# Kernel optimization log

Hardware: AMD Instinct MI355X
Metric: run time of the kernel (lower is better)

The kernel has to match this reference:

```python
import jax, jax.numpy as jnp
import numpy as np

WS = 7  # window size
EPS_COS = 1e-8
BN_EPS = 1e-5


def _third_layer_mask():
    row = np.repeat(np.arange(7), 7)[:14]
    b = np.tile(row, (7, 1))                      # (7,14) values {0,1}
    m = np.concatenate([b, b + 2], axis=0)        # (14,14) values {0,1,2,3}
    return jnp.asarray(m, dtype=jnp.int32)


def _window_partition(x, ws):
    B, C, H, W = x.shape
    x = x.reshape(B, C, H // ws, ws, W // ws, ws)
    return x.transpose(0, 2, 4, 3, 5, 1).reshape(B, (H // ws) * (W // ws), ws * ws, C)


def _windows_select(x, k):
    a0 = _window_partition(x, WS)                               # (B,nW,49,C)
    nrm = jnp.linalg.norm(a0, axis=-1)                          # (B,nW,49)
    dots = jnp.einsum('bwic,bwjc->bwij', a0, a0)
    cos = dots / jnp.maximum(nrm[..., :, None] * nrm[..., None, :], EPS_COS)
    s = jnp.triu(cos).sum(axis=(-2, -1))                        # (B,nW)
    _, idx = jax.lax.top_k(s, k)                                # (B,k)
    return idx


def _spitial_sim_weight(s):
    # s: (B, N, N) attention scores, N = 196
    B, N, _ = s.shape
    spa = jnp.mean(s, axis=-1, keepdims=True)                   # (B,N,1)
    os_spa = jnp.abs(spa - jnp.swapaxes(spa, -1, -2))           # (B,N,N)
    vals, _ = jax.lax.top_k(os_spa, N // 2)                     # descending
    last = vals[..., -1:]                                       # k-th largest, (B,N,1)
    os1f = os_spa + jnp.eye(N, dtype=s.dtype) * 10000.0
    os1 = jnp.where(os1f < last, 0.0, 1.0)
    # NOTE: original code compares the *binarized* os_spa_1 against last_value
    os2 = jnp.where(os1 > last, 0.0, 1.0)
    w1 = os1 * s
    w1 = jax.nn.softmax(jnp.where(w1 == 0, -100.0, w1), axis=-1)
    w2 = os2 * s
    w2 = jax.nn.softmax(jnp.where(w2 == 0, -100.0, w2), axis=-1)
    return w1 + w2


def _conv1x1(x, w, b):
    return jnp.einsum('bchw,oc->bohw', x, w) + b[None, :, None, None]


def _conv3x3(x, w, b):
    y = jax.lax.conv_general_dilated(x, w, (1, 1), 'SAME',
                                     dimension_numbers=('NCHW', 'OIHW', 'NCHW'))
    return y + b[None, :, None, None]


def _bn_train(x, g, beta):
    m = x.mean(axis=(0, 2, 3), keepdims=True)
    v = x.var(axis=(0, 2, 3), keepdims=True)
    return (x - m) / jnp.sqrt(v + BN_EPS) * g[None, :, None, None] + beta[None, :, None, None]


def setup_inputs() -> dict:
    key = jax.random.key(0)
    ks = jax.random.split(key, 16)
    B, C = 256, 384
    Ch = C // 4
    sc = 0.02
    return {
        'x': jax.random.normal(ks[0], (B, C, 14, 14), jnp.float32),
        'qw': jax.random.normal(ks[1], (C, C), jnp.float32) * sc,
        'qb': jnp.zeros((C,), jnp.float32),
        'kw': jax.random.normal(ks[2], (C, C), jnp.float32) * sc,
        'kb': jnp.zeros((C,), jnp.float32),
        'vw': jax.random.normal(ks[3], (C, C), jnp.float32) * sc,
        'vb': jnp.zeros((C,), jnp.float32),
        'fcw': jax.random.normal(ks[4], (C, C), jnp.float32) * sc,
        'fcb': jnp.zeros((C,), jnp.float32),
        'c1w': jax.random.normal(ks[5], (Ch, C, 3, 3), jnp.float32) * sc,
        'c1b': jnp.zeros((Ch,), jnp.float32),
        'bn1g': jnp.ones((Ch,), jnp.float32),
        'bn1b': jnp.zeros((Ch,), jnp.float32),
        'c2w': jax.random.normal(ks[6], (C, Ch, 3, 3), jnp.float32) * sc,
        'c2b': jnp.zeros((C,), jnp.float32),
        'bn2g': jnp.ones((C,), jnp.float32),
        'bn2b': jnp.zeros((C,), jnp.float32),
        'gamm': 1,
    }


def reference(x, qw, qb, kw, kb, vw, vb, fcw, fcb,
              c1w, c1b, bn1g, bn1b, c2w, c2b, bn2g, bn2b, gamm):
    B, C, H, W = x.shape
    sel = _windows_select(x, 2)                                  # (B,2) window ids
    third = _third_layer_mask()                                  # (14,14)
    member = (third[None, :, :, None] == sel[:, None, None, :]).any(-1)  # (B,14,14)
    mask = jnp.where(member, 0.0, 1.0)[:, None]                  # (B,1,14,14)
    mask1 = 1.0 - mask
    g = jnp.asarray(gamm, x.dtype)
    mask = mask.at[0].set(g)
    mask1 = mask1.at[0].set(g)

    q = _conv1x1(x * mask, qw, qb).reshape(B, C, -1).transpose(0, 2, 1)   # (B,HW,C)
    k = _conv1x1(x * mask1, kw, kb).reshape(B, C, -1).transpose(0, 2, 1)
    v = _conv1x1(x, vw, vb).reshape(B, C, -1).transpose(0, 2, 1)

    attn = jnp.einsum('bic,bjc->bij', q, k)                      # (B,196,196)
    w = _spitial_sim_weight(attn)
    feat = jnp.einsum('bij,bjc->bic', w, v)                      # (B,196,C)
    out = feat @ fcw.T + fcb
    out = out.transpose(0, 2, 1).reshape(B, 384, 14, 14)
    out = jax.nn.relu(_bn_train(_conv3x3(out, c1w, c1b), bn1g, bn1b))
    out = jax.nn.relu(_bn_train(_conv3x3(out, c2w, c2b), bn2g, bn2b))
    return out
```

## Files before the change

kernel.cpp:

```cpp
#include <hip/hip_runtime.h>

static constexpr int B_ = 256;
static constexpr int C_ = 384;
static constexpr int N_ = 196;
static constexpr int H_ = 14;
static constexpr int CH_ = 96;
static constexpr int PW_ = 49;
static constexpr int NPAIR_ = 1225;

using bf8 = __attribute__((ext_vector_type(8))) short;
using f4  = __attribute__((ext_vector_type(4))) float;

__device__ __forceinline__ float bf2f(unsigned short u) {
    unsigned int x = ((unsigned int)u) << 16;
    return __builtin_bit_cast(float, x);
}
__device__ __forceinline__ unsigned short f2bf(float f) {
    unsigned int x = __builtin_bit_cast(unsigned int, f);
    x = x + 0x7FFFu + ((x >> 16) & 1u);
    return (unsigned short)(x >> 16);
}

__global__ __launch_bounds__(256) void k_winsel(const float* __restrict__ x,
                                                float* __restrict__ swin) {
    int blk = blockIdx.x;
    int b = blk >> 2, wi = blk & 3;
    int hr = (wi >> 1) * 7, wc0 = (wi & 1) * 7;
    __shared__ float xs[128 * PW_];
    __shared__ float dots[NPAIR_];
    __shared__ float nrm[PW_];
    __shared__ float red[256];
    int tid = threadIdx.x;
    int pi[5], pj[5];
    int nm = 0;
    for (int p = tid; p < NPAIR_; p += 256) {
        int pp = p, i = 0;
        while (pp >= PW_ - i) { pp -= PW_ - i; ++i; }
        pi[nm] = i; pj[nm] = i + pp; ++nm;
    }
    float acc[5] = {0.f, 0.f, 0.f, 0.f, 0.f};
    for (int c0 = 0; c0 < C_; c0 += 128) {
        __syncthreads();
        for (int e = tid; e < 128 * PW_; e += 256) {
            int cc = e / PW_, i = e - cc * PW_;
            int h = hr + i / 7, w = wc0 + i % 7;
            xs[e] = x[((b * C_ + c0 + cc) * H_ + h) * H_ + w];
        }
        __syncthreads();
        for (int cc = 0; cc < 128; ++cc) {
            const float* row = &xs[cc * PW_];
            #pragma unroll
            for (int t = 0; t < 5; ++t)
                if (t < nm) acc[t] = fmaf(row[pi[t]], row[pj[t]], acc[t]);
        }
    }
    for (int t = 0; t < nm; ++t) dots[tid + t * 256] = acc[t];
    __syncthreads();
    if (tid < PW_) {
        int diag = tid * PW_ - tid * (tid - 1) / 2;
        nrm[tid] = sqrtf(dots[diag]);
    }
    __syncthreads();
    float part = 0.f;
    for (int t = 0; t < nm; ++t) {
        float den = fmaxf(nrm[pi[t]] * nrm[pj[t]], 1e-8f);
        part += dots[tid + t * 256] / den;
    }
    red[tid] = part;
    __syncthreads();
    for (int st = 128; st > 0; st >>= 1) {
        if (tid < st) red[tid] += red[tid + st];
        __syncthreads();
    }
    if (tid == 0) swin[blk] = red[0];
}

__global__ __launch_bounds__(256) void k_mask(const float* __restrict__ swin,
                                              const void* __restrict__ gammp,
                                              float* __restrict__ mA,
                                              float* __restrict__ mB) {
    int b = blockIdx.x;
    float sv[4];
    #pragma unroll
    for (int i = 0; i < 4; ++i) sv[i] = swin[b * 4 + i];
    int i0 = 0; float bv = sv[0];
    #pragma unroll
    for (int i = 1; i < 4; ++i) if (sv[i] > bv) { bv = sv[i]; i0 = i; }
    int i1 = -1; float bv1 = -1e30f;
    #pragma unroll
    for (int i = 0; i < 4; ++i) {
        if (i == i0) continue;
        if (sv[i] > bv1) { bv1 = sv[i]; i1 = i; }
    }
    int iv = *(const int*)gammp;
    float g = (iv == 1) ? 1.0f : __int_as_float(iv);
    int n = threadIdx.x;
    if (n < N_) {
        int h = n / 14, w = n - h * 14;
        int widx = ((h >= 7) ? 2 : 0) + ((w >= 7) ? 1 : 0);
        bool member = (widx == i0) || (widx == i1);
        float a = member ? 0.f : 1.f;
        float bm = 1.f - a;
        if (b == 0) { a = g; bm = g; }
        mA[b * N_ + n] = a;
        mB[b * N_ + n] = bm;
    }
}

__global__ __launch_bounds__(256) void k_qkv(const float* __restrict__ x,
                                             const float* __restrict__ W,
                                             const float* __restrict__ bias,
                                             const float* __restrict__ mask,
                                             float* __restrict__ out) {
    int b = blockIdx.x, n0 = blockIdx.y * 64, o0 = blockIdx.z * 64;
    __shared__ float xs[16][65];
    __shared__ float ws[64][17];
    int tid = threadIdx.x, tx = tid & 15, ty = tid >> 4;
    float acc[4][4] = {};
    for (int c0 = 0; c0 < C_; c0 += 16) {
        __syncthreads();
        for (int e = tid; e < 1024; e += 256) {
            int cc = e >> 6, nn = e & 63;
            int n = n0 + nn;
            xs[cc][nn] = (n < N_) ? x[(b * C_ + c0 + cc) * N_ + n] : 0.f;
        }
        for (int e = tid; e < 1024; e += 256) {
            int oo = e >> 4, cc = e & 15;
            ws[oo][cc] = W[(o0 + oo) * C_ + c0 + cc];
        }
        __syncthreads();
        #pragma unroll
        for (int cc = 0; cc < 16; ++cc) {
            float a[4], bb[4];
            #pragma unroll
            for (int i = 0; i < 4; ++i) a[i] = xs[cc][ty * 4 + i];
            #pragma unroll
            for (int j = 0; j < 4; ++j) bb[j] = ws[tx * 4 + j][cc];
            #pragma unroll
            for (int i = 0; i < 4; ++i)
                #pragma unroll
                for (int j = 0; j < 4; ++j) acc[i][j] = fmaf(a[i], bb[j], acc[i][j]);
        }
    }
    #pragma unroll
    for (int i = 0; i < 4; ++i) {
        int n = n0 + ty * 4 + i;
        if (n >= N_) continue;
        float m = mask ? mask[b * N_ + n] : 1.f;
        #pragma unroll
        for (int j = 0; j < 4; ++j) {
            int o = o0 + tx * 4 + j;
            out[(b * N_ + n) * C_ + o] = m * acc[i][j] + bias[o];
        }
    }
}

__global__ __launch_bounds__(256) void k_attn(const float* __restrict__ q,
                                              const float* __restrict__ k,
                                              float* __restrict__ attn) {
    int b = blockIdx.x, i0 = blockIdx.y * 64, j0 = blockIdx.z * 64;
    __shared__ float qs[64][17];
    __shared__ float ks[64][17];
    int tid = threadIdx.x, tx = tid & 15, ty = tid >> 4;
    float acc[4][4] = {};
    for (int c0 = 0; c0 < C_; c0 += 16) {
        __syncthreads();
        for (int e = tid; e < 1024; e += 256) {
            int r = e >> 4, cc = e & 15;
            int i = i0 + r;
            qs[r][cc] = (i < N_) ? q[(b * N_ + i) * C_ + c0 + cc] : 0.f;
            int j = j0 + r;
            ks[r][cc] = (j < N_) ? k[(b * N_ + j) * C_ + c0 + cc] : 0.f;
        }
        __syncthreads();
        #pragma unroll
        for (int cc = 0; cc < 16; ++cc) {
            float a[4], bb[4];
            #pragma unroll
            for (int i = 0; i < 4; ++i) a[i] = qs[ty * 4 + i][cc];
            #pragma unroll
            for (int j = 0; j < 4; ++j) bb[j] = ks[tx * 4 + j][cc];
            #pragma unroll
            for (int i = 0; i < 4; ++i)
                #pragma unroll
                for (int j = 0; j < 4; ++j) acc[i][j] = fmaf(a[i], bb[j], acc[i][j]);
        }
    }
    #pragma unroll
    for (int i = 0; i < 4; ++i) {
        int ii = i0 + ty * 4 + i;
        if (ii >= N_) continue;
        #pragma unroll
        for (int j = 0; j < 4; ++j) {
            int jj = j0 + tx * 4 + j;
            if (jj < N_) attn[(b * N_ + ii) * N_ + jj] = acc[i][j];
        }
    }
}

__global__ __launch_bounds__(256) void k_spa(const float* __restrict__ attn,
                                             float* __restrict__ spa) {
    int row = blockIdx.x;
    const float* rp = attn + (size_t)row * N_;
    int t = threadIdx.x;
    float v = (t < N_) ? rp[t] : 0.f;
    __shared__ float red[256];
    red[t] = v; __syncthreads();
    for (int st = 128; st > 0; st >>= 1) {
        if (t < st) red[t] += red[t + st];
        __syncthreads();
    }
    if (t == 0) spa[row] = red[0] / (float)N_;
}

__global__ __launch_bounds__(256) void k_weight(const float* __restrict__ attn,
                                                const float* __restrict__ spa,
                                                unsigned short* __restrict__ wbf) {
    int row = blockIdx.x;
    int b = row / N_, i = row - b * N_;
    int t = threadIdx.x;
    __shared__ float osp[N_];
    __shared__ float red[256];
    __shared__ float lastsh;
    float myspa = spa[row];
    float o = 0.f;
    if (t < N_) { o = fabsf(myspa - spa[b * N_ + t]); osp[t] = o; }
    __syncthreads();
    if (t < N_) {
        int cgt = 0, ceq = 0;
        for (int j = 0; j < N_; ++j) {
            float oj = osp[j];
            cgt += (oj > o) ? 1 : 0;
            ceq += (oj == o) ? 1 : 0;
        }
        if (cgt <= 97 && cgt + ceq >= 98) lastsh = o;
    }
    __syncthreads();
    float last = lastsh;
    const float* rowp = attn + (size_t)row * N_;
    float s = (t < N_) ? rowp[t] : 0.f;
    float a1 = -1e30f, a2 = -1e30f;
    if (t < N_) {
        float of = o + ((t == i) ? 10000.f : 0.f);
        float o1 = (of < last) ? 0.f : 1.f;
        float o2 = (o1 > last) ? 0.f : 1.f;
        float w1 = o1 * s;
        float w2 = o2 * s;
        a1 = (w1 == 0.f) ? -100.f : w1;
        a2 = (w2 == 0.f) ? -100.f : w2;
    }
    red[t] = a1; __syncthreads();
    for (int st = 128; st > 0; st >>= 1) {
        if (t < st) red[t] = fmaxf(red[t], red[t + st]);
        __syncthreads();
    }
    float m1 = red[0]; __syncthreads();
    float e1 = (t < N_) ? expf(a1 - m1) : 0.f;
    red[t] = e1; __syncthreads();
    for (int st = 128; st > 0; st >>= 1) {
        if (t < st) red[t] += red[t + st];
        __syncthreads();
    }
    float S1 = red[0]; __syncthreads();
    red[t] = a2; __syncthreads();
    for (int st = 128; st > 0; st >>= 1) {
        if (t < st) red[t] = fmaxf(red[t], red[t + st]);
        __syncthreads();
    }
    float m2 = red[0]; __syncthreads();
    float e2 = (t < N_) ? expf(a2 - m2) : 0.f;
    red[t] = e2; __syncthreads();
    for (int st = 128; st > 0; st >>= 1) {
        if (t < st) red[t] += red[t + st];
        __syncthreads();
    }
    float S2 = red[0]; __syncthreads();
    if (t < 224)
        wbf[(size_t)row * 224 + t] = (t < N_) ? f2bf(e1 / S1 + e2 / S2) : (unsigned short)0;
}

__global__ __launch_bounds__(256) void k_wprep(const float* __restrict__ c1w,
                                               const float* __restrict__ c2w,
                                               const float* __restrict__ vw,
                                               const float* __restrict__ fcw,
                                               unsigned short* __restrict__ W1p,
                                               unsigned short* __restrict__ W2p,
                                               unsigned short* __restrict__ vwb,
                                               unsigned short* __restrict__ fcwb) {
    int i = blockIdx.x * 256 + threadIdx.x;
    if (i < 331776) {
        int qt = i >> 5, k = i & 31;
        int q = qt / (9 * 96); int r = qt - q * 9 * 96;
        int tap = r / 96, o = r - tap * 96;
        W1p[i] = f2bf(c1w[(o * 384 + q * 32 + k) * 9 + tap]);
        return;
    }
    i -= 331776;
    if (i < 331776) {
        int qt = i >> 5, k = i & 31;
        int q = qt / (9 * 384); int r = qt - q * 9 * 384;
        int tap = r / 384, o = r - tap * 384;
        W2p[i] = f2bf(c2w[(o * 96 + q * 32 + k) * 9 + tap]);
        return;
    }
    i -= 331776;
    if (i < 147456) { vwb[i] = f2bf(vw[i]); return; }
    i -= 147456;
    if (i < 147456) { fcwb[i] = f2bf(fcw[i]); }
}

template <int CIN, int COUT, bool TRANS>
__global__ __launch_bounds__(256) void k_convm(
    const unsigned short* __restrict__ in,
    const unsigned short* __restrict__ Wg,
    const float* __restrict__ cb,
    const float* __restrict__ scale,
    const float* __restrict__ shift,
    unsigned short* __restrict__ outb,
    float* __restrict__ outf,
    float* __restrict__ ssum, float* __restrict__ ssq) {
    constexpr int CPT = CIN / 32;
    __shared__ unsigned short Bs[197 * 40];
    int b = blockIdx.x, o0 = blockIdx.y * 32;
    int tid = threadIdx.x, lane = tid & 63, wid = tid >> 6;
    int col = lane & 15, rowg = lane >> 4;

    if (tid < 10) *(unsigned long long*)&Bs[196 * 40 + tid * 4] = 0ull;

    int a0[4], vb[4];
    #pragma unroll
    for (int f = 0; f < 4; ++f) {
        int px = wid * 64 + f * 16 + col;
        int h = px / 14, w = px - h * 14;
        a0[f] = px * 80 + rowg * 16;
        int m = 0;
        #pragma unroll
        for (int tap = 0; tap < 9; ++tap) {
            int dh = tap / 3 - 1, dw = tap % 3 - 1;
            if (px < 196 && (unsigned)(h + dh) < 14u && (unsigned)(w + dw) < 14u)
                m |= 1 << tap;
        }
        vb[f] = m;
    }
    const int zaddr = 196 * 80 + rowg * 16;
    const int doff[9] = {-15 * 80, -14 * 80, -13 * 80, -80, 0, 80, 13 * 80, 14 * 80, 15 * 80};

    f4 acc[4][2];
    #pragma unroll
    for (int f = 0; f < 4; ++f) { acc[f][0] = (f4){0,0,0,0}; acc[f][1] = (f4){0,0,0,0}; }

    int c4 = (tid & 7) << 2, pxs = tid >> 3;
    int cpair = tid & 15, qd0 = tid >> 4;

    for (int kq = 0; kq < CPT; ++kq) {
        __syncthreads();
        if constexpr (!TRANS) {
            #pragma unroll
            for (int i = 0; i < 7; ++i) {
                int px = pxs + 32 * i;
                if (px < 196)
                    *(unsigned long long*)&Bs[px * 40 + c4] =
                        *(const unsigned long long*)&in[((size_t)b * 196 + px) * CIN + kq * 32 + c4];
            }
        } else {
            int ch = kq * 32 + 2 * cpair;
            float s0 = scale[ch], s1 = scale[ch + 1];
            float h0 = shift[ch], h1 = shift[ch + 1];
            const unsigned short* r0 = in + ((size_t)b * CIN + ch) * 196;
            const unsigned short* r1 = r0 + 196;
            #pragma unroll
            for (int qi = 0; qi < 4; ++qi) {
                int quad = qd0 + 16 * qi;
                if (quad < 49) {
                    unsigned long long ra = *(const unsigned long long*)&r0[quad * 4];
                    unsigned long long rb = *(const unsigned long long*)&r1[quad * 4];
                    #pragma unroll
                    for (int j = 0; j < 4; ++j) {
                        float v0 = fmaxf(fmaf(bf2f((unsigned short)(ra >> (16 * j))), s0, h0), 0.f);
                        float v1 = fmaxf(fmaf(bf2f((unsigned short)(rb >> (16 * j))), s1, h1), 0.f);
                        unsigned int pk = (unsigned int)f2bf(v0) | ((unsigned int)f2bf(v1) << 16);
                        *(unsigned int*)&Bs[(quad * 4 + j) * 40 + cpair * 2] = pk;
                    }
                }
            }
        }
        __syncthreads();
        #pragma unroll
        for (int tap = 0; tap < 9; ++tap) {
            const unsigned short* wp =
                Wg + ((size_t)((kq * 9 + tap) * COUT) + o0 + col) * 32 + rowg * 8;
            bf8 af0 = *(const bf8*)wp;
            bf8 af1 = *(const bf8*)(wp + 16 * 32);
            #pragma unroll
            for (int f = 0; f < 4; ++f) {
                int ba = ((vb[f] >> tap) & 1) ? a0[f] + doff[tap] : zaddr;
                bf8 bv = *(const bf8*)((const char*)Bs + ba);
                acc[f][0] = __builtin_amdgcn_mfma_f32_16x16x32_bf16(af0, bv, acc[f][0], 0, 0, 0);
                acc[f][1] = __builtin_amdgcn_mfma_f32_16x16x32_bf16(af1, bv, acc[f][1], 0, 0, 0);
            }
        }
    }

    float bias[2][4], s1a[2][4] = {}, s2a[2][4] = {};
    #pragma unroll
    for (int oh = 0; oh < 2; ++oh)
        #pragma unroll
        for (int r = 0; r < 4; ++r) bias[oh][r] = cb[o0 + oh * 16 + rowg * 4 + r];
    #pragma unroll
    for (int f = 0; f < 4; ++f) {
        int px = wid * 64 + f * 16 + col;
        bool pv = px < 196;
        #pragma unroll
        for (int oh = 0; oh < 2; ++oh)
            #pragma unroll
            for (int r = 0; r < 4; ++r) {
                float val = acc[f][oh][r] + bias[oh][r];
                if (pv) {
                    int o = o0 + oh * 16 + rowg * 4 + r;
                    if constexpr (!TRANS)
                        outb[((size_t)b * COUT + o) * 196 + px] = f2bf(val);
                    else
                        outf[((size_t)b * COUT + o) * 196 + px] = val;
                    s1a[oh][r] += val;
                    s2a[oh][r] += val * val;
                }
            }
    }
    #pragma unroll
    for (int oh = 0; oh < 2; ++oh)
        #pragma unroll
        for (int r = 0; r < 4; ++r) {
            float a = s1a[oh][r], c = s2a[oh][r];
            #pragma unroll
            for (int m = 8; m >= 1; m >>= 1) {
                a += __shfl_xor(a, m, 64);
                c += __shfl_xor(c, m, 64);
            }
            if (col == 0) {
                int o = o0 + oh * 16 + rowg * 4 + r;
                atomicAdd(&ssum[o], a);
                atomicAdd(&ssq[o], c);
            }
        }
}

template <int K, bool BIASCOL>
__global__ __launch_bounds__(256) void k_gemm_nt(
    const unsigned short* __restrict__ A,
    const unsigned short* __restrict__ Bm, long bstrB,
    const float* __restrict__ biasc,
    unsigned short* __restrict__ out) {
    __shared__ unsigned short Bs[197 * 40];
    int b = blockIdx.x, c0 = blockIdx.y * 32;
    int tid = threadIdx.x, lane = tid & 63, wid = tid >> 6;
    int col = lane & 15, rowg = lane >> 4;
    const unsigned short* Ab = A + (size_t)b * 196 * K;
    const unsigned short* Bb = Bm + (size_t)b * bstrB;

    if (tid < 10) *(unsigned long long*)&Bs[196 * 40 + tid * 4] = 0ull;
    int a0[4]; bool pv[4];
    #pragma unroll
    for (int f = 0; f < 4; ++f) {
        int px = wid * 64 + f * 16 + col;
        a0[f] = px * 80 + rowg * 16;
        pv[f] = px < 196;
    }
    const int zaddr = 196 * 80 + rowg * 16;
    f4 acc[4][2];
    #pragma unroll
    for (int f = 0; f < 4; ++f) { acc[f][0] = (f4){0,0,0,0}; acc[f][1] = (f4){0,0,0,0}; }
    int c4 = (tid & 7) << 2, pxs = tid >> 3;

    for (int kq = 0; kq < K / 32; ++kq) {
        __syncthreads();
        #pragma unroll
        for (int i = 0; i < 7; ++i) {
            int px = pxs + 32 * i;
            if (px < 196)
                *(unsigned long long*)&Bs[px * 40 + c4] =
                    *(const unsigned long long*)&Ab[(size_t)px * K + kq * 32 + c4];
        }
        __syncthreads();
        const unsigned short* bp = Bb + (size_t)(c0 + col) * K + kq * 32 + rowg * 8;
        bf8 b0 = *(const bf8*)bp;
        bf8 b1 = *(const bf8*)(bp + (size_t)16 * K);
        #pragma unroll
        for (int f = 0; f < 4; ++f) {
            int ba = pv[f] ? a0[f] : zaddr;
            bf8 av = *(const bf8*)((const char*)Bs + ba);
            acc[f][0] = __builtin_amdgcn_mfma_f32_16x16x32_bf16(av, b0, acc[f][0], 0, 0, 0);
            acc[f][1] = __builtin_amdgcn_mfma_f32_16x16x32_bf16(av, b1, acc[f][1], 0, 0, 0);
        }
    }
    float bc[2] = {0.f, 0.f};
    if constexpr (BIASCOL) { bc[0] = biasc[c0 + col]; bc[1] = biasc[c0 + 16 + col]; }
    #pragma unroll
    for (int f = 0; f < 4; ++f) {
        #pragma unroll
        for (int oh = 0; oh < 2; ++oh)
            #pragma unroll
            for (int r = 0; r < 4; ++r) {
                int m = wid * 64 + f * 16 + rowg * 4 + r;
                if (m < 196)
                    out[((size_t)b * 196 + m) * 384 + c0 + oh * 16 + col] =
                        f2bf(acc[f][oh][r] + bc[oh]);
            }
    }
}

__global__ __launch_bounds__(256) void k_gemm_v(
    const float* __restrict__ x,
    const unsigned short* __restrict__ vwb,
    const float* __restrict__ vbias,
    unsigned short* __restrict__ vt) {
    __shared__ unsigned short Bs[197 * 40];
    int b = blockIdx.x, o0 = blockIdx.y * 32;
    int tid = threadIdx.x, lane = tid & 63, wid = tid >> 6;
    int col = lane & 15, rowg = lane >> 4;

    if (tid < 10) *(unsigned long long*)&Bs[196 * 40 + tid * 4] = 0ull;
    int a0[4]; bool pv[4];
    #pragma unroll
    for (int f = 0; f < 4; ++f) {
        int px = wid * 64 + f * 16 + col;
        a0[f] = px * 80 + rowg * 16;
        pv[f] = px < 196;
    }
    const int zaddr = 196 * 80 + rowg * 16;
    f4 acc[4][2];
    #pragma unroll
    for (int f = 0; f < 4; ++f) { acc[f][0] = (f4){0,0,0,0}; acc[f][1] = (f4){0,0,0,0}; }
    int cpair = tid & 15, qd0 = tid >> 4;

    for (int kq = 0; kq < 12; ++kq) {
        __syncthreads();
        const float* r0 = x + ((size_t)b * 384 + kq * 32 + 2 * cpair) * 196;
        const float* r1 = r0 + 196;
        #pragma unroll
        for (int qi = 0; qi < 4; ++qi) {
            int quad = qd0 + 16 * qi;
            if (quad < 49) {
                float4 ra = *(const float4*)&r0[quad * 4];
                float4 rb = *(const float4*)&r1[quad * 4];
                float av[4] = {ra.x, ra.y, ra.z, ra.w};
                float bv[4] = {rb.x, rb.y, rb.z, rb.w};
                #pragma unroll
                for (int j = 0; j < 4; ++j) {
                    unsigned int pk = (unsigned int)f2bf(av[j]) | ((unsigned int)f2bf(bv[j]) << 16);
                    *(unsigned int*)&Bs[(quad * 4 + j) * 40 + cpair * 2] = pk;
                }
            }
        }
        __syncthreads();
        const unsigned short* wp = vwb + (size_t)(o0 + col) * 384 + kq * 32 + rowg * 8;
        bf8 w0 = *(const bf8*)wp;
        bf8 w1 = *(const bf8*)(wp + 16 * 384);
        #pragma unroll
        for (int f = 0; f < 4; ++f) {
            int ba = pv[f] ? a0[f] : zaddr;
            bf8 av = *(const bf8*)((const char*)Bs + ba);
            acc[f][0] = __builtin_amdgcn_mfma_f32_16x16x32_bf16(w0, av, acc[f][0], 0, 0, 0);
            acc[f][1] = __builtin_amdgcn_mfma_f32_16x16x32_bf16(w1, av, acc[f][1], 0, 0, 0);
        }
    }
    float bia[2][4];
    #pragma unroll
    for (int oh = 0; oh < 2; ++oh)
        #pragma unroll
        for (int r = 0; r < 4; ++r) bia[oh][r] = vbias[o0 + oh * 16 + rowg * 4 + r];
    #pragma unroll
    for (int f = 0; f < 4; ++f) {
        int n = wid * 64 + f * 16 + col;
        if (n >= 224) continue;
        #pragma unroll
        for (int oh = 0; oh < 2; ++oh)
            #pragma unroll
            for (int r = 0; r < 4; ++r) {
                int o = o0 + oh * 16 + rowg * 4 + r;
                vt[((size_t)b * 384 + o) * 224 + n] =
                    (n < 196) ? f2bf(acc[f][oh][r] + bia[oh][r]) : (unsigned short)0;
            }
    }
}

__global__ __launch_bounds__(256) void k_zero(float* __restrict__ p, int n) {
    int i = blockIdx.x * 256 + threadIdx.x;
    if (i < n) p[i] = 0.f;
}
__global__ __launch_bounds__(256) void k_bnfin(const float* __restrict__ ssum,
                                               const float* __restrict__ ssq,
                                               const float* __restrict__ g,
                                               const float* __restrict__ beta,
                                               float* __restrict__ scale,
                                               float* __restrict__ shift, int C) {
    int c = blockIdx.x * 256 + threadIdx.x;
    if (c >= C) return;
    float M = (float)(B_ * N_);
    float mean = ssum[c] / M;
    float var = ssq[c] / M - mean * mean;
    float sc = g[c] / sqrtf(var + 1e-5f);
    scale[c] = sc;
    shift[c] = beta[c] - mean * sc;
}

__global__ __launch_bounds__(256) void k_final(float* __restrict__ buf,
                                               const float* __restrict__ scale,
                                               const float* __restrict__ shift) {
    size_t total = (size_t)B_ * C_ * N_;
    for (size_t idx = (size_t)blockIdx.x * 256 + threadIdx.x; idx < total;
         idx += (size_t)gridDim.x * 256) {
        int c = (int)((idx / N_) % C_);
        buf[idx] = fmaxf(buf[idx] * scale[c] + shift[c], 0.f);
    }
}

extern "C" void kernel_launch(void* const* d_in, const int* in_sizes, int n_in,
                              void* d_out, int out_size, void* d_ws, size_t ws_size,
                              hipStream_t stream) {
    (void)in_sizes; (void)n_in; (void)out_size;
    const float* x    = (const float*)d_in[0];
    const float* qw   = (const float*)d_in[1];
    const float* qb   = (const float*)d_in[2];
    const float* kw   = (const float*)d_in[3];
    const float* kb   = (const float*)d_in[4];
    const float* vw   = (const float*)d_in[5];
    const float* vb   = (const float*)d_in[6];
    const float* fcw  = (const float*)d_in[7];
    const float* fcb  = (const float*)d_in[8];
    const float* c1w  = (const float*)d_in[9];
    const float* c1b  = (const float*)d_in[10];
    const float* bn1g = (const float*)d_in[11];
    const float* bn1b = (const float*)d_in[12];
    const float* c2w  = (const float*)d_in[13];
    const float* c2b  = (const float*)d_in[14];
    const float* bn2g = (const float*)d_in[15];
    const float* bn2b = (const float*)d_in[16];
    const void*  gam  = d_in[17];

    const size_t WSF = ws_size / sizeof(float);
    const size_t F_Y1 = 2408448;
    const size_t F_W1 = 165888, F_W2 = 165888, F_VW = 73728, F_FW = 73728;
    const size_t F_MA = 50176, F_MB = 50176, F_SW = 1024, F_ST = 1920;
    const size_t fixedF = F_Y1 + F_W1 + F_W2 + F_VW + F_FW + F_MA + F_MB + F_SW + F_ST + 512;
    const size_t perB = 75264 + 75264 + 38416 + 196 + 21952 + 43008 + 37632 + 37632 + 64;
    const int tiers[7] = {64, 32, 16, 8, 4, 2, 1};
    int GB = 1;
    for (int t = 0; t < 7; ++t) {
        if (fixedF + (size_t)tiers[t] * perB <= WSF) { GB = tiers[t]; break; }
    }

    float* wsf = (float*)d_ws;
    size_t off = 0;
    unsigned short* y1   = (unsigned short*)(wsf + off); off += F_Y1;
    unsigned short* W1p  = (unsigned short*)(wsf + off); off += F_W1;
    unsigned short* W2p  = (unsigned short*)(wsf + off); off += F_W2;
    unsigned short* vwb  = (unsigned short*)(wsf + off); off += F_VW;
    unsigned short* fcwb = (unsigned short*)(wsf + off); off += F_FW;
    float* mA   = wsf + off; off += F_MA;
    float* mB   = wsf + off; off += F_MB;
    float* swin = wsf + off; off += F_SW;
    float* stats = wsf + off; off += F_ST + 512;
    float* ssum1 = stats,         *ssq1 = stats + 96;
    float* ssum2 = stats + 192,   *ssq2 = stats + 576;
    float* scale1 = stats + 960,  *shift1 = stats + 1056;
    float* scale2 = stats + 1152, *shift2 = stats + 1536;
    float* qh    = wsf + off; off += (size_t)GB * 75264;
    float* kh    = wsf + off; off += (size_t)GB * 75264;
    float* attnh = wsf + off; off += (size_t)GB * 38416;
    float* spah  = wsf + off; off += (size_t)GB * 196 + 64;
    unsigned short* wbf   = (unsigned short*)(wsf + off); off += (size_t)GB * 21952;
    unsigned short* vt    = (unsigned short*)(wsf + off); off += (size_t)GB * 43008;
    unsigned short* featb = (unsigned short*)(wsf + off); off += (size_t)GB * 37632;
    unsigned short* fcoutg = (unsigned short*)(wsf + off); off += (size_t)GB * 37632;

    float* yout = (float*)d_out;

    k_zero<<<dim3(4), 256, 0, stream>>>(stats, 960);
    k_wprep<<<dim3(3744), 256, 0, stream>>>(c1w, c2w, vw, fcw, W1p, W2p, vwb, fcwb);
    k_winsel<<<dim3(B_ * 4), 256, 0, stream>>>(x, swin);
    k_mask<<<dim3(B_), 256, 0, stream>>>(swin, gam, mA, mB);

    for (int b0 = 0; b0 < B_; b0 += GB) {
        const float* xg = x + (size_t)b0 * C_ * N_;
        k_qkv<<<dim3(GB, 4, 6), 256, 0, stream>>>(xg, qw, qb, mA + (size_t)b0 * N_, qh);
        k_qkv<<<dim3(GB, 4, 6), 256, 0, stream>>>(xg, kw, kb, mB + (size_t)b0 * N_, kh);
        k_attn<<<dim3(GB, 4, 4), 256, 0, stream>>>(qh, kh, attnh);
        k_spa<<<dim3(GB * N_), 256, 0, stream>>>(attnh, spah);
        k_weight<<<dim3(GB * N_), 256, 0, stream>>>(attnh, spah, wbf);
        k_gemm_v<<<dim3(GB, 12), 256, 0, stream>>>(xg, vwb, vb, vt);
        k_gemm_nt<224, false><<<dim3(GB, 12), 256, 0, stream>>>(
            wbf, vt, 86016L, nullptr, featb);
        k_gemm_nt<384, true><<<dim3(GB, 12), 256, 0, stream>>>(
            featb, fcwb, 0L, fcb, fcoutg);
        k_convm<384, 96, false><<<dim3(GB, 3), 256, 0, stream>>>(
            fcoutg, W1p, c1b, nullptr, nullptr,
            y1 + (size_t)b0 * CH_ * N_, nullptr, ssum1, ssq1);
    }
    k_bnfin<<<dim3(1), 256, 0, stream>>>(ssum1, ssq1, bn1g, bn1b, scale1, shift1, 96);
    k_convm<96, 384, true><<<dim3(B_, 12), 256, 0, stream>>>(
        y1, W2p, c2b, scale1, shift1, nullptr, yout, ssum2, ssq2);
    k_bnfin<<<dim3(2), 256, 0, stream>>>(ssum2, ssq2, bn2g, bn2b, scale2, shift2, 384);
    k_final<<<dim3(18816), 256, 0, stream>>>(yout, scale2, shift2);
}
```

Measured before the change: 2.851 ms.

## Stage conv weights in LDS and batch conv1 over all images

The conv kernel now copies each k-slice of weights for all 9 taps into shared memory once per block instead of having every wave read them from global memory. The host also reserves a full-batch buffer for the fc output when workspace allows. With that buffer, the first 3x3 conv runs once over all 256 images instead of per group with few blocks, which should fix low occupancy on small grids. The cost is extra LDS per block and a large workspace buffer, with the old per-group path kept as a fallback.

Result: faster. 2.730 ms (-4.3%).

```diff
diff --git a/kernel.cpp b/kernel.cpp
--- a/kernel.cpp
+++ b/kernel.cpp
@@ -321,6 +321,7 @@
     float* __restrict__ ssum, float* __restrict__ ssq) {
     constexpr int CPT = CIN / 32;
     __shared__ unsigned short Bs[197 * 40];
+    __shared__ unsigned short As[9 * 32 * 36];
     int b = blockIdx.x, o0 = blockIdx.y * 32;
     int tid = threadIdx.x, lane = tid & 63, wid = tid >> 6;
     int col = lane & 15, rowg = lane >> 4;
@@ -354,6 +355,12 @@
 
     for (int kq = 0; kq < CPT; ++kq) {
         __syncthreads();
+        for (int u = tid; u < 1152; u += 256) {
+            int r = u >> 2, part = u & 3;
+            int tap = r >> 5, o = r & 31;
+            *(int4*)&As[r * 36 + part * 8] =
+                *(const int4*)&Wg[((size_t)((kq * 9 + tap) * COUT) + o0 + o) * 32 + part * 8];
+        }
         if constexpr (!TRANS) {
             #pragma unroll
             for (int i = 0; i < 7; ++i) {
@@ -387,10 +394,8 @@
         __syncthreads();
         #pragma unroll
         for (int tap = 0; tap < 9; ++tap) {
-            const unsigned short* wp =
-                Wg + ((size_t)((kq * 9 + tap) * COUT) + o0 + col) * 32 + rowg * 8;
-            bf8 af0 = *(const bf8*)wp;
-            bf8 af1 = *(const bf8*)(wp + 16 * 32);
+            bf8 af0 = *(const bf8*)&As[(tap * 32 + col) * 36 + rowg * 8];
+            bf8 af1 = *(const bf8*)&As[(tap * 32 + 16 + col) * 36 + rowg * 8];
             #pragma unroll
             for (int f = 0; f < 4; ++f) {
                 int ba = ((vb[f] >> tap) & 1) ? a0[f] + doff[tap] : zaddr;
@@ -641,12 +646,19 @@
     const size_t F_Y1 = 2408448;
     const size_t F_W1 = 165888, F_W2 = 165888, F_VW = 73728, F_FW = 73728;
     const size_t F_MA = 50176, F_MB = 50176, F_SW = 1024, F_ST = 1920;
-    const size_t fixedF = F_Y1 + F_W1 + F_W2 + F_VW + F_FW + F_MA + F_MB + F_SW + F_ST + 512;
-    const size_t perB = 75264 + 75264 + 38416 + 196 + 21952 + 43008 + 37632 + 37632 + 64;
+    const size_t F_FC = 9633792;
+    const size_t fixedC = F_Y1 + F_W1 + F_W2 + F_VW + F_FW + F_MA + F_MB + F_SW + F_ST + 512;
+    const size_t perA = 75264 + 75264 + 38416 + 196 + 64 + 21952 + 43008 + 37632;
+    const size_t perBf = perA + 37632;
     const int tiers[7] = {64, 32, 16, 8, 4, 2, 1};
-    int GB = 1;
+    int GB = 0; bool modeA = false;
     for (int t = 0; t < 7; ++t) {
-        if (fixedF + (size_t)tiers[t] * perB <= WSF) { GB = tiers[t]; break; }
+        if (fixedC + F_FC + (size_t)tiers[t] * perA <= WSF) { GB = tiers[t]; modeA = true; break; }
+    }
+    if (!modeA) {
+        for (int t = 0; t < 7; ++t)
+            if (fixedC + (size_t)tiers[t] * perBf <= WSF) { GB = tiers[t]; break; }
+        if (GB == 0) GB = 1;
     }
 
     float* wsf = (float*)d_ws;
@@ -664,6 +676,8 @@
     float* ssum2 = stats + 192,   *ssq2 = stats + 576;
     float* scale1 = stats + 960,  *shift1 = stats + 1056;
     float* scale2 = stats + 1152, *shift2 = stats + 1536;
+    unsigned short* fcfull = nullptr;
+    if (modeA) { fcfull = (unsigned short*)(wsf + off); off += F_FC; }
     float* qh    = wsf + off; off += (size_t)GB * 75264;
     float* kh    = wsf + off; off += (size_t)GB * 75264;
     float* attnh = wsf + off; off += (size_t)GB * 38416;
@@ -671,7 +685,8 @@
     unsigned short* wbf   = (unsigned short*)(wsf + off); off += (size_t)GB * 21952;
     unsigned short* vt    = (unsigned short*)(wsf + off); off += (size_t)GB * 43008;
     unsigned short* featb = (unsigned short*)(wsf + off); off += (size_t)GB * 37632;
-    unsigned short* fcoutg = (unsigned short*)(wsf + off); off += (size_t)GB * 37632;
+    unsigned short* fcoutg = nullptr;
+    if (!modeA) { fcoutg = (unsigned short*)(wsf + off); off += (size_t)GB * 37632; }
 
     float* yout = (float*)d_out;
 
@@ -690,11 +705,18 @@
         k_gemm_v<<<dim3(GB, 12), 256, 0, stream>>>(xg, vwb, vb, vt);
         k_gemm_nt<224, false><<<dim3(GB, 12), 256, 0, stream>>>(
             wbf, vt, 86016L, nullptr, featb);
+        unsigned short* fdst = modeA ? (fcfull + (size_t)b0 * 75264) : fcoutg;
         k_gemm_nt<384, true><<<dim3(GB, 12), 256, 0, stream>>>(
-            featb, fcwb, 0L, fcb, fcoutg);
-        k_convm<384, 96, false><<<dim3(GB, 3), 256, 0, stream>>>(
-            fcoutg, W1p, c1b, nullptr, nullptr,
-            y1 + (size_t)b0 * CH_ * N_, nullptr, ssum1, ssq1);
+            featb, fcwb, 0L, fcb, fdst);
+        if (!modeA) {
+            k_convm<384, 96, false><<<dim3(GB, 3), 256, 0, stream>>>(
+                fcoutg, W1p, c1b, nullptr, nullptr,
+                y1 + (size_t)b0 * CH_ * N_, nullptr, ssum1, ssq1);
+        }
+    }
+    if (modeA) {
+        k_convm<384, 96, false><<<dim3(B_, 3), 256, 0, stream>>>(
+            fcfull, W1p, c1b, nullptr, nullptr, y1, nullptr, ssum1, ssq1);
     }
     k_bnfin<<<dim3(1), 256, 0, stream>>>(ssum1, ssq1, bn1g, bn1b, scale1, shift1, 96);
     k_convm<96, 384, true><<<dim3(B_, 12), 256, 0, stream>>>(
```
